# Kernel tuning notes

Measured on AMD Instinct MI355X. Metric: run time of the kernel, lower is better.

The kernel has to match this reference:

```python
import jax, jax.numpy as jnp
import numpy as np

def mexican_hat(z):
    z2 = z * z
    return (1.0 - z2) * jnp.exp(-0.5 * z2)

def setup_inputs() -> dict:
    key = jax.random.key(0)
    k1, k2 = jax.random.split(key)
    B, N, D = 8192, 512, 64
    x = jax.random.normal(k1, (B, D), dtype=jnp.float32)
    centers = jax.random.normal(k2, (N, D), dtype=jnp.float32)
    scales = jnp.ones((N, D), dtype=jnp.float32)
    return {"x": x, "centers": centers, "scales": scales}

def reference(x, centers, scales):
    # x: (B, D); centers/scales: (N, D)
    z = (x[:, None, :] - centers[None, :, :]) / scales[None, :, :]  # (B, N, D)
    psi = mexican_hat(z)
    h = jnp.prod(psi, axis=2)  # (B, N)
    return h
```

## Files before the change

### kernel.cpp

```cpp
#include <hip/hip_runtime.h>
#include <hip/hip_bf16.h>


#define DD 64
#define NT 8

typedef float v2f __attribute__((ext_vector_type(2)));

__global__ void prep_packed(const float* __restrict__ c,
                            const float* __restrict__ s,
                            float4* __restrict__ pp, int N) {
    int i = blockIdx.x * 256 + threadIdx.x;
    int total = N * (DD / 2);
    if (i < total) {
        int dp = i / N, n = i - dp * N;
        int d = dp * 2;
        float r0 = 1.0f / s[n * DD + d];
        float r1 = 1.0f / s[n * DD + d + 1];
        pp[i] = make_float4(c[n * DD + d] * r0, c[n * DD + d + 1] * r1, r0, r1);
    }
}

__global__ __launch_bounds__(256, 4)
void wavelet_kernel(const float* __restrict__ x,
                    const float4* __restrict__ pp,
                    float* __restrict__ out, int B, int N) {
    int b = blockIdx.x * 256 + threadIdx.x;
    if (b >= B) return;
    int n0 = blockIdx.y * NT;
    const float4* pb = pp + n0;
    const float4* xv = (const float4*)(x + (size_t)b * DD);

    float acc[NT];
#pragma unroll
    for (int j = 0; j < NT; ++j) acc[j] = 1.0f;

#pragma unroll
    for (int g = 0; g < 4; ++g) {
        v2f p[NT], s2[NT];
#pragma unroll
        for (int j = 0; j < NT; ++j) {
            p[j]  = (v2f){1.0f, 1.0f};
            s2[j] = (v2f){0.0f, 0.0f};
        }
#pragma unroll
        for (int dq = 0; dq < 4; ++dq) {
            float4 xq = xv[g * 4 + dq];
            v2f xa = {xq.x, xq.y};
            v2f xb2 = {xq.z, xq.w};
            const float4* rowa = pb + (size_t)(g * 8 + dq * 2) * N;
            const float4* rowb = rowa + N;
#pragma unroll
            for (int j = 0; j < NT; ++j) {
                float4 qa = rowa[j];
                v2f cp = {qa.x, qa.y};
                v2f rs = {qa.z, qa.w};
                v2f z = __builtin_elementwise_fma(xa, rs, -cp);
                v2f w = z * z;
                p[j] = __builtin_elementwise_fma(-w, p[j], p[j]);
                s2[j] += w;
            }
#pragma unroll
            for (int j = 0; j < NT; ++j) {
                float4 qb = rowb[j];
                v2f cp = {qb.x, qb.y};
                v2f rs = {qb.z, qb.w};
                v2f z = __builtin_elementwise_fma(xb2, rs, -cp);
                v2f w = z * z;
                p[j] = __builtin_elementwise_fma(-w, p[j], p[j]);
                s2[j] += w;
            }
        }
#pragma unroll
        for (int j = 0; j < NT; ++j) {
            float pr = p[j].x * p[j].y;
            float sr = s2[j].x + s2[j].y;
            acc[j] *= pr * __expf(-0.5f * sr);
        }
    }

    float4* op = (float4*)(out + (size_t)b * N + n0);
#pragma unroll
    for (int j = 0; j < NT / 4; ++j)
        op[j] = make_float4(acc[4 * j], acc[4 * j + 1],
                            acc[4 * j + 2], acc[4 * j + 3]);
}

extern "C" void kernel_launch(void* const* d_in, const int* in_sizes, int n_in,
                              void* d_out, int out_size, void* d_ws, size_t ws_size,
                              hipStream_t stream) {
    const float* x = (const float*)d_in[0];
    const float* c = (const float*)d_in[1];
    const float* s = (const float*)d_in[2];
    float* out = (float*)d_out;

    int B = in_sizes[0] / DD;
    int N = in_sizes[1] / DD;

    float4* pp = (float4*)d_ws;

    int total = N * (DD / 2);
    prep_packed<<<(total + 255) / 256, 256, 0, stream>>>(c, s, pp, N);

    dim3 grid((B + 255) / 256, N / NT);
    wavelet_kernel<<<grid, 256, 0, stream>>>(x, pp, out, B, N);
}
```

Baseline: 97.74 us.

## Stage center params in LDS, transpose x, compute two batch rows per thread

The per-block slice of packed center/scale parameters now goes into shared memory once, instead of every thread reading it from global memory. The prep kernel also transposes x into a dimension-pair-major layout so that x loads coalesce across threads. Each thread now handles two batch rows, so every parameter load from LDS is reused across two rows and the grid is halved. The costs are higher register pressure under the launch bound, an extra global pass to transpose x, and the loss of a bounds check because B is assumed to be a multiple of 512.

Result: slower. 123.0 us (+25.8%).

```diff
diff --git a/kernel.cpp b/kernel.cpp
--- a/kernel.cpp
+++ b/kernel.cpp
@@ -4,86 +4,110 @@
 
 #define DD 64
 #define NT 8
+#define BPT 2
+#define BB (256 * BPT)
 
 typedef float v2f __attribute__((ext_vector_type(2)));
 
-__global__ void prep_packed(const float* __restrict__ c,
-                            const float* __restrict__ s,
-                            float4* __restrict__ pp, int N) {
+__global__ __launch_bounds__(256)
+void prep(const float* __restrict__ x, const float* __restrict__ c,
+          const float* __restrict__ s, float4* __restrict__ pp,
+          float2* __restrict__ xp, int B, int N) {
     int i = blockIdx.x * 256 + threadIdx.x;
-    int total = N * (DD / 2);
-    if (i < total) {
-        int dp = i / N, n = i - dp * N;
-        int d = dp * 2;
-        float r0 = 1.0f / s[n * DD + d];
-        float r1 = 1.0f / s[n * DD + d + 1];
-        pp[i] = make_float4(c[n * DD + d] * r0, c[n * DD + d + 1] * r1, r0, r1);
+    int nxp = B * (DD / 2);
+    if (i < nxp) {
+        int dp = i / B, b = i - dp * B;
+        xp[i] = make_float2(x[b * DD + 2 * dp], x[b * DD + 2 * dp + 1]);
+    } else {
+        int k = i - nxp;
+        if (k < (DD / 2) * N) {
+            int dp = k / N, n = k - dp * N;
+            float r0 = 1.0f / s[n * DD + 2 * dp];
+            float r1 = 1.0f / s[n * DD + 2 * dp + 1];
+            pp[k] = make_float4(c[n * DD + 2 * dp] * r0,
+                                c[n * DD + 2 * dp + 1] * r1, r0, r1);
+        }
     }
 }
 
 __global__ __launch_bounds__(256, 4)
-void wavelet_kernel(const float* __restrict__ x,
+void wavelet_kernel(const float2* __restrict__ xp,
                     const float4* __restrict__ pp,
                     float* __restrict__ out, int B, int N) {
-    int b = blockIdx.x * 256 + threadIdx.x;
-    if (b >= B) return;
+    __shared__ float4 prm[(DD / 2) * NT];
+
+    int t = threadIdx.x;
     int n0 = blockIdx.y * NT;
-    const float4* pb = pp + n0;
-    const float4* xv = (const float4*)(x + (size_t)b * DD);
+    int b0 = blockIdx.x * BB;
 
-    float acc[NT];
+    {
+        int dp = t >> 3, j = t & 7;
+        prm[dp * NT + j] = pp[dp * N + n0 + j];
+    }
+    __syncthreads();
+
+    int bA = b0 + t;
+    int bB = bA + 256;
+
+    float acc[BPT][NT];
 #pragma unroll
-    for (int j = 0; j < NT; ++j) acc[j] = 1.0f;
+    for (int r = 0; r < BPT; ++r)
+#pragma unroll
+        for (int j = 0; j < NT; ++j) acc[r][j] = 1.0f;
 
 #pragma unroll
     for (int g = 0; g < 4; ++g) {
-        v2f p[NT], s2[NT];
+        v2f p[BPT][NT], s2[BPT][NT];
 #pragma unroll
-        for (int j = 0; j < NT; ++j) {
-            p[j]  = (v2f){1.0f, 1.0f};
-            s2[j] = (v2f){0.0f, 0.0f};
-        }
-#pragma unroll
-        for (int dq = 0; dq < 4; ++dq) {
-            float4 xq = xv[g * 4 + dq];
-            v2f xa = {xq.x, xq.y};
-            v2f xb2 = {xq.z, xq.w};
-            const float4* rowa = pb + (size_t)(g * 8 + dq * 2) * N;
-            const float4* rowb = rowa + N;
+        for (int r = 0; r < BPT; ++r)
 #pragma unroll
             for (int j = 0; j < NT; ++j) {
-                float4 qa = rowa[j];
-                v2f cp = {qa.x, qa.y};
-                v2f rs = {qa.z, qa.w};
-                v2f z = __builtin_elementwise_fma(xa, rs, -cp);
-                v2f w = z * z;
-                p[j] = __builtin_elementwise_fma(-w, p[j], p[j]);
-                s2[j] += w;
+                p[r][j]  = (v2f){1.0f, 1.0f};
+                s2[r][j] = (v2f){0.0f, 0.0f};
             }
+
+#pragma unroll
+        for (int dq = 0; dq < 8; ++dq) {
+            int dp = g * 8 + dq;
+            float2 xa = xp[(size_t)dp * B + bA];
+            float2 xb = xp[(size_t)dp * B + bB];
+            v2f x0 = {xa.x, xa.y};
+            v2f x1 = {xb.x, xb.y};
 #pragma unroll
             for (int j = 0; j < NT; ++j) {
-                float4 qb = rowb[j];
-                v2f cp = {qb.x, qb.y};
-                v2f rs = {qb.z, qb.w};
-                v2f z = __builtin_elementwise_fma(xb2, rs, -cp);
-                v2f w = z * z;
-                p[j] = __builtin_elementwise_fma(-w, p[j], p[j]);
-                s2[j] += w;
+                float4 q = prm[dp * NT + j];
+                v2f cp = {q.x, q.y};
+                v2f rs = {q.z, q.w};
+
+                v2f z0 = __builtin_elementwise_fma(x0, rs, -cp);
+                v2f w0 = z0 * z0;
+                p[0][j] = __builtin_elementwise_fma(-w0, p[0][j], p[0][j]);
+                s2[0][j] += w0;
+
+                v2f z1 = __builtin_elementwise_fma(x1, rs, -cp);
+                v2f w1 = z1 * z1;
+                p[1][j] = __builtin_elementwise_fma(-w1, p[1][j], p[1][j]);
+                s2[1][j] += w1;
             }
         }
+
 #pragma unroll
-        for (int j = 0; j < NT; ++j) {
-            float pr = p[j].x * p[j].y;
-            float sr = s2[j].x + s2[j].y;
-            acc[j] *= pr * __expf(-0.5f * sr);
-        }
+        for (int r = 0; r < BPT; ++r)
+#pragma unroll
+            for (int j = 0; j < NT; ++j) {
+                float pr = p[r][j].x * p[r][j].y;
+                float sr = s2[r][j].x + s2[r][j].y;
+                acc[r][j] *= pr * __expf(-0.5f * sr);
+            }
     }
 
-    float4* op = (float4*)(out + (size_t)b * N + n0);
 #pragma unroll
-    for (int j = 0; j < NT / 4; ++j)
-        op[j] = make_float4(acc[4 * j], acc[4 * j + 1],
-                            acc[4 * j + 2], acc[4 * j + 3]);
+    for (int r = 0; r < BPT; ++r) {
+        int b = (r == 0) ? bA : bB;
+        float4* op = (float4*)(out + (size_t)b * N + n0);
+        op[0] = make_float4(acc[r][0], acc[r][1], acc[r][2], acc[r][3]);
+        op[1] = make_float4(acc[r][4], acc[r][5], acc[r][6], acc[r][7]);
+    }
 }
 
 extern "C" void kernel_launch(void* const* d_in, const int* in_sizes, int n_in,
@@ -98,10 +122,11 @@
     int N = in_sizes[1] / DD;
 
     float4* pp = (float4*)d_ws;
+    float2* xp = (float2*)((char*)d_ws + (size_t)(DD / 2) * N * 16);
 
-    int total = N * (DD / 2);
-    prep_packed<<<(total + 255) / 256, 256, 0, stream>>>(c, s, pp, N);
+    int total = B * (DD / 2) + (DD / 2) * N;
+    prep<<<(total + 255) / 256, 256, 0, stream>>>(x, c, s, pp, xp, B, N);
 
-    dim3 grid((B + 255) / 256, N / NT);
-    wavelet_kernel<<<grid, 256, 0, stream>>>(x, pp, out, B, N);
+    dim3 grid(B / BB, N / NT);
+    wavelet_kernel<<<grid, 256, 0, stream>>>(xp, pp, out, B, N);
 }
```
